# Performance work log

Hardware: AMD Instinct MI355X
Metric: run time of the kernel (lower is better)

The kernel has to match this reference:

```python
import jax, jax.numpy as jnp
import numpy as np
import math

B, N, D_MODEL = 1, 2925, 1536
NUM_HEADS, HEAD_DIM = 12, 128
F, H, W = 13, 15, 15
MAX_SEQ = 1024
EPS = 1e-6


def _make_freqs(max_seq, dim):
    # (cos, sin) pairs for half-dim rotary frequencies, base 10000
    inv = 1.0 / (10000.0 ** (np.arange(0, dim, 2, dtype=np.float64) / dim))
    ang = np.arange(max_seq, dtype=np.float64)[:, None] * inv[None, :]
    return jnp.asarray(np.stack([np.cos(ang), np.sin(ang)], axis=-1), dtype=jnp.float32)


def setup_inputs() -> dict:
    key = jax.random.key(0)
    ks = jax.random.split(key, 10)
    s = 1.0 / math.sqrt(D_MODEL)
    dim_base = HEAD_DIM // 6              # 21
    dim_t = HEAD_DIM - 4 * dim_base       # 44
    dim_h = 2 * dim_base                  # 42
    return {
        "x": jax.random.normal(ks[0], (B, N, D_MODEL), dtype=jnp.float32),
        "Wq": jax.random.normal(ks[1], (D_MODEL, D_MODEL), dtype=jnp.float32) * s,
        "bq": jnp.zeros((D_MODEL,), dtype=jnp.float32),
        "Wk": jax.random.normal(ks[2], (D_MODEL, D_MODEL), dtype=jnp.float32) * s,
        "bk": jnp.zeros((D_MODEL,), dtype=jnp.float32),
        "Wv": jax.random.normal(ks[3], (D_MODEL, D_MODEL), dtype=jnp.float32) * s,
        "bv": jnp.zeros((D_MODEL,), dtype=jnp.float32),
        "Wo": jax.random.normal(ks[4], (D_MODEL, D_MODEL), dtype=jnp.float32) * s,
        "bo": jnp.zeros((D_MODEL,), dtype=jnp.float32),
        "q_scale": jnp.ones((D_MODEL,), dtype=jnp.float32),
        "k_scale": jnp.ones((D_MODEL,), dtype=jnp.float32),
        "freqs_t": _make_freqs(MAX_SEQ, dim_t),
        "freqs_h": _make_freqs(MAX_SEQ, dim_h),
        "freqs_w": _make_freqs(MAX_SEQ, dim_h),
        "f": F, "h": H, "w": W,
    }


def _rms_norm(x, scale, eps=EPS):
    var = jnp.mean(jnp.square(x), axis=-1, keepdims=True)
    return x * jax.lax.rsqrt(var + eps) * scale


def _rope_apply(x, f, h, w, freqs_t, freqs_h, freqs_w):
    # x: [b, n, H, D] with n == f*h*w
    b, n, nh, d = x.shape
    db = d // 6
    dt, dh, dw = d - 4 * db, 2 * db, 2 * db
    ft = jnp.broadcast_to(freqs_t[:f, None, None, :, :], (f, h, w, dt // 2, 2))
    fh = jnp.broadcast_to(freqs_h[None, :h, None, :, :], (f, h, w, dh // 2, 2))
    fw = jnp.broadcast_to(freqs_w[None, None, :w, :, :], (f, h, w, dw // 2, 2))
    fg = jnp.concatenate([ft, fh, fw], axis=3).reshape(n, d // 2, 2)[None, :, None, :, :]
    xc = x.reshape(b, n, nh, d // 2, 2)
    re = xc[..., 0] * fg[..., 0] - xc[..., 1] * fg[..., 1]
    im = xc[..., 0] * fg[..., 1] + xc[..., 1] * fg[..., 0]
    return jnp.stack([re, im], axis=-1).reshape(b, n, nh, d)


def reference(x, Wq, bq, Wk, bk, Wv, bv, Wo, bo, q_scale, k_scale,
              freqs_t, freqs_h, freqs_w, f, h, w):
    b, n, _ = x.shape
    nh, d = NUM_HEADS, HEAD_DIM
    # projections + RMSNorm across full hidden dim (before head split)
    q = _rms_norm(x @ Wq + bq, q_scale).reshape(b, n, nh, d)
    k = _rms_norm(x @ Wk + bk, k_scale).reshape(b, n, nh, d)
    v = (x @ Wv + bv).reshape(b, n, nh, d)
    # 3D RoPE on [b, n, H, D] layout
    q = _rope_apply(q, f, h, w, freqs_t, freqs_h, freqs_w)
    k = _rope_apply(k, f, h, w, freqs_t, freqs_h, freqs_w)
    # [b, H, n, d]
    q = q.transpose(0, 2, 1, 3)
    k = k.transpose(0, 2, 1, 3)
    v = v.transpose(0, 2, 1, 3)
    scores = jnp.einsum("bhid,bhjd->bhij", q, k) / math.sqrt(d)
    attn = jax.nn.softmax(scores, axis=-1)
    out = jnp.einsum("bhij,bhjd->bhid", attn, v)
    out = out.transpose(0, 2, 1, 3).reshape(b, n, nh * d)
    return out @ Wo + bo
```

## Files before the change

### kernel.cpp

```cpp
#include <hip/hip_runtime.h>


#define N_TOK 2925
#define DMODEL 1536
#define NHEAD 12
#define HDIM 128
#define KSPLIT 1472
#define VT_STRIDE 2944

typedef __attribute__((ext_vector_type(8))) __bf16 bf16x8;
typedef __attribute__((ext_vector_type(4))) float floatx4;

#define MFMA(a, b, c) __builtin_amdgcn_mfma_f32_16x16x32_bf16((a), (b), (c), 0, 0, 0)

static __device__ __forceinline__ unsigned short f2bf(float f) {
    unsigned u = __builtin_bit_cast(unsigned, f);
    return (unsigned short)((u + 0x7fffu + ((u >> 16) & 1u)) >> 16);
}

static __device__ __forceinline__ void gload_lds16(const unsigned short* g, unsigned short* l) {
    __builtin_amdgcn_global_load_lds((const __attribute__((address_space(1))) void*)g,
                                     (__attribute__((address_space(3))) void*)l, 16, 0, 0);
}

__global__ __launch_bounds__(256) void k_convert_x(const float* __restrict__ x,
                                                   unsigned short* __restrict__ xb, int n) {
    int i = (blockIdx.x * 256 + threadIdx.x) * 4;
    if (i < n) {
        float4 v = *(const float4*)(x + i);
        uint2 o;
        o.x = (unsigned)f2bf(v.x) | ((unsigned)f2bf(v.y) << 16);
        o.y = (unsigned)f2bf(v.z) | ((unsigned)f2bf(v.w) << 16);
        *(uint2*)(xb + i) = o;
    }
}

__global__ __launch_bounds__(256) void k_transpose_w(const float* __restrict__ W0,
                                                     const float* __restrict__ W1,
                                                     const float* __restrict__ W2,
                                                     const float* __restrict__ W3,
                                                     unsigned short* __restrict__ Wt) {
    __shared__ float tile[32][33];
    const float* W = blockIdx.z == 0 ? W0 : blockIdx.z == 1 ? W1 : blockIdx.z == 2 ? W2 : W3;
    unsigned short* out = Wt + (size_t)blockIdx.z * DMODEL * DMODEL;
    int tx = threadIdx.x, ty = threadIdx.y;
    int bx = blockIdx.x * 32, by = blockIdx.y * 32;
#pragma unroll
    for (int i = 0; i < 4; i++)
        tile[ty + 8 * i][tx] = W[(size_t)(by + ty + 8 * i) * DMODEL + bx + tx];
    __syncthreads();
#pragma unroll
    for (int i = 0; i < 4; i++)
        out[(size_t)(bx + ty + 8 * i) * DMODEL + by + tx] = f2bf(tile[tx][ty + 8 * i]);
}

__global__ __launch_bounds__(256, 2) void k_gemm(const unsigned short* __restrict__ A,
                                                 const unsigned short* __restrict__ BtBase,
                                                 const float* __restrict__ b0,
                                                 const float* __restrict__ b1,
                                                 const float* __restrict__ b2,
                                                 float* __restrict__ Cbase, int M) {
    const int z = blockIdx.z;
    const unsigned short* Bt = BtBase + (size_t)z * DMODEL * DMODEL;
    const float* bias = (z == 0) ? b0 : (z == 1) ? b1 : b2;
    float* C = Cbase + (size_t)z * M * DMODEL;

    __shared__ __align__(16) unsigned short As[128 * 32];
    __shared__ __align__(16) unsigned short Bs[128 * 32];

    const int tid = threadIdx.x;
    const int wave = tid >> 6, lane = tid & 63, quad = lane >> 4, l16 = lane & 15;
    const int wr = wave >> 1, wc = wave & 1;
    const int m0 = blockIdx.y * 128, n0 = blockIdx.x * 128;

    const int r4 = tid >> 2, c4 = (tid & 3) * 8;

    floatx4 acc[4][4] = {};

    for (int k0 = 0; k0 < DMODEL; k0 += 32) {
        gload_lds16(A + (size_t)(m0 + r4) * DMODEL + k0 + c4,       &As[r4 * 32 + c4]);
        gload_lds16(A + (size_t)(m0 + r4 + 64) * DMODEL + k0 + c4,  &As[(r4 + 64) * 32 + c4]);
        gload_lds16(Bt + (size_t)(n0 + r4) * DMODEL + k0 + c4,      &Bs[r4 * 32 + c4]);
        gload_lds16(Bt + (size_t)(n0 + r4 + 64) * DMODEL + k0 + c4, &Bs[(r4 + 64) * 32 + c4]);
        __syncthreads();

        bf16x8 af[4], bfm[4];
#pragma unroll
        for (int i = 0; i < 4; i++)
            af[i] = *(const bf16x8*)&As[(wr * 64 + i * 16 + l16) * 32 + quad * 8];
#pragma unroll
        for (int j = 0; j < 4; j++)
            bfm[j] = *(const bf16x8*)&Bs[(wc * 64 + j * 16 + l16) * 32 + quad * 8];
#pragma unroll
        for (int i = 0; i < 4; i++)
#pragma unroll
            for (int j = 0; j < 4; j++)
                acc[i][j] = MFMA(af[i], bfm[j], acc[i][j]);
        __syncthreads();
    }

#pragma unroll
    for (int j = 0; j < 4; j++) {
        int cg = n0 + wc * 64 + j * 16 + l16;
        float bv = bias[cg];
#pragma unroll
        for (int i = 0; i < 4; i++) {
            int rbase = m0 + wr * 64 + i * 16 + quad * 4;
#pragma unroll
            for (int r = 0; r < 4; r++) {
                int rg = rbase + r;
                if (rg < M) C[(size_t)rg * DMODEL + cg] = acc[i][j][r] + bv;
            }
        }
    }
}

__global__ __launch_bounds__(256) void k_norm_rope(const float* __restrict__ Qf,
                                                   const float* __restrict__ Kf,
                                                   const float* __restrict__ Vf,
                                                   const float* __restrict__ qsc,
                                                   const float* __restrict__ ksc,
                                                   const float* __restrict__ ft,
                                                   const float* __restrict__ fh,
                                                   const float* __restrict__ fw,
                                                   unsigned short* __restrict__ qb,
                                                   unsigned short* __restrict__ kb,
                                                   unsigned short* __restrict__ vb) {
    const int n = blockIdx.x;
    const int tid = threadIdx.x, wave = tid >> 6, lane = tid & 63;
    const int t_i = n / 225, rem = n % 225, h_i = rem / 15, w_i = rem % 15;
    const float att_scale = 0.08838834764831845f * 1.4426950408889634f;

    float2 qv[3], kv[3], vv[3];
    float sq = 0.f, sk = 0.f;
#pragma unroll
    for (int c = 0; c < 3; c++) {
        int p = tid + 256 * c;
        qv[c] = *(const float2*)(Qf + (size_t)n * DMODEL + 2 * p);
        kv[c] = *(const float2*)(Kf + (size_t)n * DMODEL + 2 * p);
        vv[c] = *(const float2*)(Vf + (size_t)n * DMODEL + 2 * p);
        sq += qv[c].x * qv[c].x + qv[c].y * qv[c].y;
        sk += kv[c].x * kv[c].x + kv[c].y * kv[c].y;
    }
#pragma unroll
    for (int off = 32; off >= 1; off >>= 1) {
        sq += __shfl_xor(sq, off, 64);
        sk += __shfl_xor(sk, off, 64);
    }
    __shared__ float red[2][4];
    if (lane == 0) { red[0][wave] = sq; red[1][wave] = sk; }
    __syncthreads();
    sq = red[0][0] + red[0][1] + red[0][2] + red[0][3];
    sk = red[1][0] + red[1][1] + red[1][2] + red[1][3];
    const float rq = rsqrtf(sq * (1.f / 1536.f) + 1e-6f) * att_scale;
    const float rk = rsqrtf(sk * (1.f / 1536.f) + 1e-6f);

#pragma unroll
    for (int c = 0; c < 3; c++) {
        int p = tid + 256 * c;
        int hd = p >> 6, pl = p & 63, dd = 2 * pl;
        float cs, sn;
        if (pl < 22)      { cs = ft[t_i * 44 + 2 * pl];        sn = ft[t_i * 44 + 2 * pl + 1]; }
        else if (pl < 43) { int pp = pl - 22; cs = fh[h_i * 42 + 2 * pp]; sn = fh[h_i * 42 + 2 * pp + 1]; }
        else              { int pp = pl - 43; cs = fw[w_i * 42 + 2 * pp]; sn = fw[w_i * 42 + 2 * pp + 1]; }
        int hidx = hd * 128 + dd;
        float q0 = qv[c].x * rq * qsc[hidx], q1 = qv[c].y * rq * qsc[hidx + 1];
        float k0 = kv[c].x * rk * ksc[hidx], k1 = kv[c].y * rk * ksc[hidx + 1];
        size_t o = ((size_t)hd * N_TOK + n) * HDIM + dd;
        unsigned qo = (unsigned)f2bf(q0 * cs - q1 * sn) | ((unsigned)f2bf(q0 * sn + q1 * cs) << 16);
        unsigned ko = (unsigned)f2bf(k0 * cs - k1 * sn) | ((unsigned)f2bf(k0 * sn + k1 * cs) << 16);
        unsigned vo = (unsigned)f2bf(vv[c].x) | ((unsigned)f2bf(vv[c].y) << 16);
        *(unsigned*)(qb + o) = qo;
        *(unsigned*)(kb + o) = ko;
        *(unsigned*)(vb + o) = vo;
    }
}

__global__ __launch_bounds__(256) void k_transpose_v(const unsigned short* __restrict__ vbi,
                                                     unsigned short* __restrict__ vt) {
    __shared__ unsigned short tile[32][33];
    const int head = blockIdx.z;
    const int t0 = blockIdx.x * 32, d0 = blockIdx.y * 32;
    const int tx = threadIdx.x, ty = threadIdx.y;
#pragma unroll
    for (int i = 0; i < 4; i++) {
        int t = t0 + ty + 8 * i;
        tile[ty + 8 * i][tx] = (t < N_TOK) ? vbi[((size_t)head * N_TOK + t) * HDIM + d0 + tx] : 0;
    }
    __syncthreads();
    int t = t0 + tx;
#pragma unroll
    for (int i = 0; i < 4; i++)
        vt[((size_t)head * HDIM + d0 + ty + 8 * i) * VT_STRIDE + t] = tile[tx][ty + 8 * i];
}

__global__ __launch_bounds__(256, 4) void k_attn_part(const unsigned short* __restrict__ qb,
                                                      const unsigned short* __restrict__ kb,
                                                      const unsigned short* __restrict__ vt,
                                                      float* __restrict__ Opart,
                                                      float* __restrict__ mbuf,
                                                      float* __restrict__ lbuf) {
    __shared__ __align__(16) unsigned short Ks[64 * 128];
    __shared__ __align__(16) unsigned short Vs[128 * 64];
    __shared__ __align__(16) unsigned short Ps[4][16 * 64];

    const int tid = threadIdx.x, wave = tid >> 6, lane = tid & 63;
    const int quad = lane >> 4, l16 = lane & 15, x7 = l16 & 7;
    const int head = blockIdx.y, z = blockIdx.z;
    const int q0 = blockIdx.x * 64 + wave * 16;
    const unsigned short* qh = qb + (size_t)head * N_TOK * HDIM;
    const unsigned short* kh = kb + (size_t)head * N_TOK * HDIM;
    const unsigned short* vh = vt + (size_t)head * HDIM * VT_STRIDE;
    unsigned short* ps = Ps[wave];

    const int kbeg = z ? KSPLIT : 0;
    const int kend = z ? N_TOK : KSPLIT;

    int koff[4];
#pragma unroll
    for (int ks = 0; ks < 4; ks++) {
        int c = ks * 4 + quad;
        koff[ks] = ((c & 8) | ((c & 7) ^ x7)) * 8;
    }
    const int pwq = (quad >> 1), pwh = (quad & 1) * 4;

    const int krow = tid >> 4, ksw = tid & 15;
    const int kc = (ksw & 8) | ((ksw & 7) ^ (krow & 7));
    const int vd = tid >> 3, vsw = tid & 7;
    const int vc = vsw ^ (vd & 7);
    const unsigned short* ksrc = kh + (size_t)krow * HDIM + kc * 8;
    const unsigned short* vsrc = vh + (size_t)vd * VT_STRIDE + vc * 8;

    bf16x8 aq[4];
    {
        int qrow = q0 + l16;
        if (qrow < N_TOK) {
#pragma unroll
            for (int ks = 0; ks < 4; ks++)
                aq[ks] = *(const bf16x8*)&qh[(size_t)qrow * HDIM + ks * 32 + quad * 8];
        } else {
#pragma unroll
            for (int ks = 0; ks < 4; ks++) aq[ks] = (bf16x8)(__bf16)0.0f;
        }
    }

    floatx4 oacc[8] = {};
    float m_l = -1e30f;
    float l_l = 0.f;

    for (int kb0 = kbeg; kb0 < kend; kb0 += 64) {
        const bool fullt = (kb0 + 64 <= kend);

        if (fullt) {
#pragma unroll
            for (int i = 0; i < 4; i++)
                gload_lds16(ksrc + (size_t)(kb0 + 16 * i) * HDIM, &Ks[(tid + 256 * i) * 8]);
        } else {
#pragma unroll
            for (int i = 0; i < 4; i++) {
                int gk = kb0 + krow + 16 * i;
                gk = gk < N_TOK ? gk : N_TOK - 1;
                gload_lds16(kh + (size_t)gk * HDIM + kc * 8, &Ks[(tid + 256 * i) * 8]);
            }
        }
#pragma unroll
        for (int i = 0; i < 4; i++)
            gload_lds16(vsrc + (size_t)(32 * i) * VT_STRIDE + kb0, &Vs[(tid + 256 * i) * 8]);
        __syncthreads();

        floatx4 sa[4] = {};
#pragma unroll
        for (int j = 0; j < 4; j++)
#pragma unroll
            for (int ks = 0; ks < 4; ks++) {
                bf16x8 bkf = *(const bf16x8*)&Ks[(j * 16 + l16) * HDIM + koff[ks]];
                sa[j] = MFMA(bkf, aq[ks], sa[j]);
            }

        float mt;
        if (fullt) {
            float m01 = fmaxf(fmaxf(sa[0][0], sa[0][1]), fmaxf(sa[0][2], sa[0][3]));
            float m23 = fmaxf(fmaxf(sa[1][0], sa[1][1]), fmaxf(sa[1][2], sa[1][3]));
            float m45 = fmaxf(fmaxf(sa[2][0], sa[2][1]), fmaxf(sa[2][2], sa[2][3]));
            float m67 = fmaxf(fmaxf(sa[3][0], sa[3][1]), fmaxf(sa[3][2], sa[3][3]));
            mt = fmaxf(fmaxf(m01, m23), fmaxf(m45, m67));
        } else {
            mt = -1e30f;
            const int kq = kb0 + quad * 4;
#pragma unroll
            for (int j = 0; j < 4; j++)
#pragma unroll
                for (int r = 0; r < 4; r++)
                    mt = fmaxf(mt, (kq + j * 16 + r < kend) ? sa[j][r] : -1e30f);
        }
        mt = fmaxf(mt, __shfl_xor(mt, 16));
        mt = fmaxf(mt, __shfl_xor(mt, 32));

        if (__any(mt > m_l + 8.f)) {
            float mn = fmaxf(m_l, mt);
            float alpha = exp2f(m_l - mn);
            m_l = mn;
            l_l *= alpha;
#pragma unroll
            for (int r = 0; r < 4; r++) {
                float ar = __shfl(alpha, quad * 4 + r, 16);
#pragma unroll
                for (int jd = 0; jd < 8; jd++) oacc[jd][r] *= ar;
            }
        }

        if (fullt) {
#pragma unroll
            for (int j = 0; j < 4; j++) {
                float p0 = exp2f(sa[j][0] - m_l), p1 = exp2f(sa[j][1] - m_l);
                float p2 = exp2f(sa[j][2] - m_l), p3 = exp2f(sa[j][3] - m_l);
                l_l += (p0 + p1) + (p2 + p3);
                uint2 w;
                w.x = (unsigned)__builtin_bit_cast(unsigned short, (__bf16)p0) |
                      ((unsigned)__builtin_bit_cast(unsigned short, (__bf16)p1) << 16);
                w.y = (unsigned)__builtin_bit_cast(unsigned short, (__bf16)p2) |
                      ((unsigned)__builtin_bit_cast(unsigned short, (__bf16)p3) << 16);
                *(uint2*)&ps[l16 * 64 + (((j * 2 + pwq) ^ x7) << 3) + pwh] = w;
            }
        } else {
            const int kq = kb0 + quad * 4;
#pragma unroll
            for (int j = 0; j < 4; j++) {
                float p[4];
#pragma unroll
                for (int r = 0; r < 4; r++) {
                    p[r] = (kq + j * 16 + r < kend) ? exp2f(sa[j][r] - m_l) : 0.f;
                    l_l += p[r];
                }
                uint2 w;
                w.x = (unsigned)__builtin_bit_cast(unsigned short, (__bf16)p[0]) |
                      ((unsigned)__builtin_bit_cast(unsigned short, (__bf16)p[1]) << 16);
                w.y = (unsigned)__builtin_bit_cast(unsigned short, (__bf16)p[2]) |
                      ((unsigned)__builtin_bit_cast(unsigned short, (__bf16)p[3]) << 16);
                *(uint2*)&ps[l16 * 64 + (((j * 2 + pwq) ^ x7) << 3) + pwh] = w;
            }
        }

#pragma unroll
        for (int ks = 0; ks < 2; ks++) {
            bf16x8 ap = *(const bf16x8*)&ps[l16 * 64 + koff[ks]];
#pragma unroll
            for (int jd = 0; jd < 8; jd++) {
                bf16x8 bvf = *(const bf16x8*)&Vs[(jd * 16 + l16) * 64 + koff[ks]];
                oacc[jd] = MFMA(ap, bvf, oacc[jd]);
            }
        }
        __syncthreads();
    }

    l_l += __shfl_xor(l_l, 16);
    l_l += __shfl_xor(l_l, 32);

#pragma unroll
    for (int r = 0; r < 4; r++) {
        int rg = q0 + quad * 4 + r;
        if (rg < N_TOK) {
            size_t rbase = ((size_t)(z * NHEAD + head) * N_TOK + rg) * HDIM;
#pragma unroll
            for (int jd = 0; jd < 8; jd++)
                Opart[rbase + jd * 16 + l16] = oacc[jd][r];
        }
    }
    if (quad == 0 && q0 + l16 < N_TOK) {
        int mi = (z * NHEAD + head) * N_TOK + q0 + l16;
        mbuf[mi] = m_l;
        lbuf[mi] = l_l;
    }
}

__global__ __launch_bounds__(256) void k_combine(const float* __restrict__ Opart,
                                                 const float* __restrict__ mbuf,
                                                 const float* __restrict__ lbuf,
                                                 unsigned short* __restrict__ ab) {
    const int R = NHEAD * N_TOK;
    int r = blockIdx.x * 8 + (threadIdx.x >> 5);
    if (r >= R) return;
    int l32 = threadIdx.x & 31;
    float m0 = mbuf[r], m1 = mbuf[R + r];
    float l0 = lbuf[r], l1 = lbuf[R + r];
    float m = fmaxf(m0, m1);
    float w0 = exp2f(m0 - m), w1 = exp2f(m1 - m);
    float inv = 1.f / (l0 * w0 + l1 * w1);
    w0 *= inv; w1 *= inv;
    float4 a = *(const float4*)&Opart[(size_t)r * HDIM + l32 * 4];
    float4 b = *(const float4*)&Opart[((size_t)R + r) * HDIM + l32 * 4];
    int head = r / N_TOK, tok = r % N_TOK;
    unsigned short* o = ab + (size_t)tok * DMODEL + head * HDIM + l32 * 4;
    uint2 pk;
    pk.x = (unsigned)f2bf(a.x * w0 + b.x * w1) | ((unsigned)f2bf(a.y * w0 + b.y * w1) << 16);
    pk.y = (unsigned)f2bf(a.z * w0 + b.z * w1) | ((unsigned)f2bf(a.w * w0 + b.w * w1) << 16);
    *(uint2*)o = pk;
}

extern "C" void kernel_launch(void* const* d_in, const int* in_sizes, int n_in,
                              void* d_out, int out_size, void* d_ws, size_t ws_size,
                              hipStream_t stream) {
    const float* x   = (const float*)d_in[0];
    const float* Wq  = (const float*)d_in[1];
    const float* bq  = (const float*)d_in[2];
    const float* Wk  = (const float*)d_in[3];
    const float* bk  = (const float*)d_in[4];
    const float* Wv  = (const float*)d_in[5];
    const float* bv  = (const float*)d_in[6];
    const float* Wo  = (const float*)d_in[7];
    const float* bo  = (const float*)d_in[8];
    const float* qsc = (const float*)d_in[9];
    const float* ksc = (const float*)d_in[10];
    const float* ft  = (const float*)d_in[11];
    const float* fh  = (const float*)d_in[12];
    const float* fw  = (const float*)d_in[13];

    char* ws = (char*)d_ws;
    unsigned short* xb   = (unsigned short*)ws; ws += (size_t)N_TOK * DMODEL * 2;
    unsigned short* Wt   = (unsigned short*)ws; ws += (size_t)4 * DMODEL * DMODEL * 2;
    unsigned short* ab   = (unsigned short*)ws; ws += (size_t)N_TOK * DMODEL * 2;
    char* qkvf_region    = ws;                  ws += (size_t)3 * N_TOK * DMODEL * 4;
    unsigned short* qkvb = (unsigned short*)ws; ws += (size_t)3 * N_TOK * DMODEL * 2;

    float* Qf = (float*)qkvf_region;
    float* Kf = Qf + (size_t)N_TOK * DMODEL;
    float* Vf = Qf + (size_t)2 * N_TOK * DMODEL;
    float* Opart = (float*)qkvf_region;
    float* mbuf  = Opart + (size_t)2 * NHEAD * N_TOK * HDIM;
    float* lbuf  = mbuf + (size_t)2 * NHEAD * N_TOK;
    unsigned short* vtp = (unsigned short*)(lbuf + (size_t)2 * NHEAD * N_TOK);

    unsigned short* qbp = qkvb;
    unsigned short* kbp = qkvb + (size_t)N_TOK * DMODEL;
    unsigned short* vbp = qkvb + (size_t)2 * N_TOK * DMODEL;

    const int nelem = N_TOK * DMODEL;
    k_convert_x<<<(nelem / 4 + 255) / 256, 256, 0, stream>>>(x, xb, nelem);
    k_transpose_w<<<dim3(48, 48, 4), dim3(32, 8), 0, stream>>>(Wq, Wk, Wv, Wo, Wt);
    k_gemm<<<dim3(12, 23, 3), 256, 0, stream>>>(xb, Wt, bq, bk, bv, Qf, N_TOK);
    k_norm_rope<<<N_TOK, 256, 0, stream>>>(Qf, Kf, Vf, qsc, ksc, ft, fh, fw, qbp, kbp, vbp);
    k_transpose_v<<<dim3(92, 4, NHEAD), dim3(32, 8), 0, stream>>>(vbp, vtp);
    k_attn_part<<<dim3(46, NHEAD, 2), 256, 0, stream>>>(qbp, kbp, vtp, Opart, mbuf, lbuf);
    k_combine<<<(NHEAD * N_TOK + 7) / 8, 256, 0, stream>>>(Opart, mbuf, lbuf, ab);
    k_gemm<<<dim3(12, 23, 1), 256, 0, stream>>>(ab, Wt + (size_t)3 * DMODEL * DMODEL,
                                                bo, bo, bo, (float*)d_out, N_TOK);
}
```

Baseline: 368.7 us.

## Overlap K/V tile loads with compute in attention and remap block order

Restructures the attention loop so the next K tile is fetched into LDS right after the QK MFMAs and the next V tile right after the PV MFMAs. Uses explicit vmcnt waits and split barriers in place of full __syncthreads, so global-to-LDS latency overlaps with softmax and MFMA work. It also remaps the linear block index so that consecutive blocks spread across heads and key splits, and raises wave priority around the MFMA sections. The risk is fragile hand-written waitcnt and barrier logic that could race or serialize.

New measurement: 368.2 us. About the same (-0.1%).

```diff
diff --git a/kernel.cpp b/kernel.cpp
--- a/kernel.cpp
+++ b/kernel.cpp
@@ -204,10 +204,15 @@
     __shared__ __align__(16) unsigned short Vs[128 * 64];
     __shared__ __align__(16) unsigned short Ps[4][16 * 64];
 
+    const int b = blockIdx.x + 46 * (blockIdx.y + 12 * (int)blockIdx.z);
+    const int w = (b & 7) * 138 + (b >> 3);
+    const int qblk = w % 46;
+    const int head = (w / 46) % 12;
+    const int z    = w / 552;
+
     const int tid = threadIdx.x, wave = tid >> 6, lane = tid & 63;
     const int quad = lane >> 4, l16 = lane & 15, x7 = l16 & 7;
-    const int head = blockIdx.y, z = blockIdx.z;
-    const int q0 = blockIdx.x * 64 + wave * 16;
+    const int q0 = qblk * 64 + wave * 16;
     const unsigned short* qh = qb + (size_t)head * N_TOK * HDIM;
     const unsigned short* kh = kb + (size_t)head * N_TOK * HDIM;
     const unsigned short* vh = vt + (size_t)head * HDIM * VT_STRIDE;
@@ -215,6 +220,7 @@
 
     const int kbeg = z ? KSPLIT : 0;
     const int kend = z ? N_TOK : KSPLIT;
+    const int ntile = (kend - kbeg + 63) >> 6;
 
     int koff[4];
 #pragma unroll
@@ -248,27 +254,36 @@
     float m_l = -1e30f;
     float l_l = 0.f;
 
-    for (int kb0 = kbeg; kb0 < kend; kb0 += 64) {
-        const bool fullt = (kb0 + 64 <= kend);
-
-        if (fullt) {
+    {
+        const bool part0 = (kbeg + 64 > kend);
+        if (!part0) {
 #pragma unroll
             for (int i = 0; i < 4; i++)
-                gload_lds16(ksrc + (size_t)(kb0 + 16 * i) * HDIM, &Ks[(tid + 256 * i) * 8]);
+                gload_lds16(ksrc + (size_t)(kbeg + 16 * i) * HDIM, &Ks[(tid + 256 * i) * 8]);
         } else {
 #pragma unroll
             for (int i = 0; i < 4; i++) {
-                int gk = kb0 + krow + 16 * i;
+                int gk = kbeg + krow + 16 * i;
                 gk = gk < N_TOK ? gk : N_TOK - 1;
                 gload_lds16(kh + (size_t)gk * HDIM + kc * 8, &Ks[(tid + 256 * i) * 8]);
             }
         }
 #pragma unroll
         for (int i = 0; i < 4; i++)
-            gload_lds16(vsrc + (size_t)(32 * i) * VT_STRIDE + kb0, &Vs[(tid + 256 * i) * 8]);
-        __syncthreads();
+            gload_lds16(vsrc + (size_t)(32 * i) * VT_STRIDE + kbeg, &Vs[(tid + 256 * i) * 8]);
+    }
+
+    for (int t = 0; t < ntile; t++) {
+        const int kb0 = kbeg + t * 64;
+        const bool fullt = (kb0 + 64 <= kend);
+        const bool has_next = (t + 1 < ntile);
+
+        asm volatile("s_waitcnt vmcnt(4)" ::: "memory");
+        __builtin_amdgcn_sched_barrier(0);
+        __builtin_amdgcn_s_barrier();
 
         floatx4 sa[4] = {};
+        __builtin_amdgcn_s_setprio(1);
 #pragma unroll
         for (int j = 0; j < 4; j++)
 #pragma unroll
@@ -276,6 +291,24 @@
                 bf16x8 bkf = *(const bf16x8*)&Ks[(j * 16 + l16) * HDIM + koff[ks]];
                 sa[j] = MFMA(bkf, aq[ks], sa[j]);
             }
+        __builtin_amdgcn_s_setprio(0);
+        __builtin_amdgcn_s_barrier();
+
+        if (has_next) {
+            const int kn = kb0 + 64;
+            if (kn + 64 <= kend) {
+#pragma unroll
+                for (int i = 0; i < 4; i++)
+                    gload_lds16(ksrc + (size_t)(kn + 16 * i) * HDIM, &Ks[(tid + 256 * i) * 8]);
+            } else {
+#pragma unroll
+                for (int i = 0; i < 4; i++) {
+                    int gk = kn + krow + 16 * i;
+                    gk = gk < N_TOK ? gk : N_TOK - 1;
+                    gload_lds16(kh + (size_t)gk * HDIM + kc * 8, &Ks[(tid + 256 * i) * 8]);
+                }
+            }
+        }
 
         float mt;
         if (fullt) {
@@ -315,12 +348,12 @@
                 float p0 = exp2f(sa[j][0] - m_l), p1 = exp2f(sa[j][1] - m_l);
                 float p2 = exp2f(sa[j][2] - m_l), p3 = exp2f(sa[j][3] - m_l);
                 l_l += (p0 + p1) + (p2 + p3);
-                uint2 w;
-                w.x = (unsigned)__builtin_bit_cast(unsigned short, (__bf16)p0) |
-                      ((unsigned)__builtin_bit_cast(unsigned short, (__bf16)p1) << 16);
-                w.y = (unsigned)__builtin_bit_cast(unsigned short, (__bf16)p2) |
-                      ((unsigned)__builtin_bit_cast(unsigned short, (__bf16)p3) << 16);
-                *(uint2*)&ps[l16 * 64 + (((j * 2 + pwq) ^ x7) << 3) + pwh] = w;
+                uint2 wv;
+                wv.x = (unsigned)__builtin_bit_cast(unsigned short, (__bf16)p0) |
+                       ((unsigned)__builtin_bit_cast(unsigned short, (__bf16)p1) << 16);
+                wv.y = (unsigned)__builtin_bit_cast(unsigned short, (__bf16)p2) |
+                       ((unsigned)__builtin_bit_cast(unsigned short, (__bf16)p3) << 16);
+                *(uint2*)&ps[l16 * 64 + (((j * 2 + pwq) ^ x7) << 3) + pwh] = wv;
             }
         } else {
             const int kq = kb0 + quad * 4;
@@ -332,15 +365,21 @@
                     p[r] = (kq + j * 16 + r < kend) ? exp2f(sa[j][r] - m_l) : 0.f;
                     l_l += p[r];
                 }
-                uint2 w;
-                w.x = (unsigned)__builtin_bit_cast(unsigned short, (__bf16)p[0]) |
-                      ((unsigned)__builtin_bit_cast(unsigned short, (__bf16)p[1]) << 16);
-                w.y = (unsigned)__builtin_bit_cast(unsigned short, (__bf16)p[2]) |
-                      ((unsigned)__builtin_bit_cast(unsigned short, (__bf16)p[3]) << 16);
-                *(uint2*)&ps[l16 * 64 + (((j * 2 + pwq) ^ x7) << 3) + pwh] = w;
-            }
-        }
-
+                uint2 wv;
+                wv.x = (unsigned)__builtin_bit_cast(unsigned short, (__bf16)p[0]) |
+                       ((unsigned)__builtin_bit_cast(unsigned short, (__bf16)p[1]) << 16);
+                wv.y = (unsigned)__builtin_bit_cast(unsigned short, (__bf16)p[2]) |
+                       ((unsigned)__builtin_bit_cast(unsigned short, (__bf16)p[3]) << 16);
+                *(uint2*)&ps[l16 * 64 + (((j * 2 + pwq) ^ x7) << 3) + pwh] = wv;
+            }
+        }
+
+        if (has_next) { asm volatile("s_waitcnt vmcnt(4)" ::: "memory"); }
+        else          { asm volatile("s_waitcnt vmcnt(0)" ::: "memory"); }
+        __builtin_amdgcn_sched_barrier(0);
+        __builtin_amdgcn_s_barrier();
+
+        __builtin_amdgcn_s_setprio(1);
 #pragma unroll
         for (int ks = 0; ks < 2; ks++) {
             bf16x8 ap = *(const bf16x8*)&ps[l16 * 64 + koff[ks]];
@@ -350,7 +389,15 @@
                 oacc[jd] = MFMA(ap, bvf, oacc[jd]);
             }
         }
-        __syncthreads();
+        __builtin_amdgcn_s_setprio(0);
+        __builtin_amdgcn_s_barrier();
+
+        if (has_next) {
+            const int kn = kb0 + 64;
+#pragma unroll
+            for (int i = 0; i < 4; i++)
+                gload_lds16(vsrc + (size_t)(32 * i) * VT_STRIDE + kn, &Vs[(tid + 256 * i) * 8]);
+        }
     }
 
     l_l += __shfl_xor(l_l, 16);
```
